# Performance work log

Hardware: AMD Instinct MI355X
Metric: run time of the kernel (lower is better)

## Reference

```python
import jax, jax.numpy as jnp
import numpy as np
import math

B, T, D, H = 4, 2048, 1024, 16
DH = D // H

def setup_inputs() -> dict:
    key = jax.random.key(0)
    ks = jax.random.split(key, 5)
    scale = 1.0 / math.sqrt(D)
    x = jax.random.normal(ks[0], (B, T, D), dtype=jnp.float32)
    Wq = jax.random.normal(ks[1], (D, D), dtype=jnp.float32) * scale
    Wk = jax.random.normal(ks[2], (D, D), dtype=jnp.float32) * scale
    Wv = jax.random.normal(ks[3], (D, D), dtype=jnp.float32) * scale
    Wo = jax.random.normal(ks[4], (D, D), dtype=jnp.float32) * scale
    mask = jnp.tril(jnp.ones((T, T), dtype=jnp.int32))  # causal, 1=keep
    return {"x": x, "mask": mask, "Wq": Wq, "Wk": Wk, "Wv": Wv, "Wo": Wo}

def reference(x, mask, Wq, Wk, Wv, Wo):
    Bx, Tx, Dx = x.shape
    # nn.Linear(bias=False): y = x @ W.T
    q = (x @ Wq.T).reshape(Bx, Tx, H, DH).transpose(0, 2, 1, 3)  # [B,H,T,dh]
    k = (x @ Wk.T).reshape(Bx, Tx, H, DH).transpose(0, 2, 1, 3)
    v = (x @ Wv.T).reshape(Bx, Tx, H, DH).transpose(0, 2, 1, 3)
    scores = jnp.einsum('bhqd,bhkd->bhqk', q, k) / math.sqrt(DH)
    m = mask[None, None, :, :]  # [1,1,T,T]
    scores = scores + (m == 0).astype(scores.dtype) * -1e9
    attn = jax.nn.softmax(scores, axis=-1)  # stable (max-subtract) like original
    out = jnp.einsum('bhqk,bhkd->bhqd', attn, v)
    out = out.transpose(0, 2, 1, 3).reshape(Bx, Tx, Dx)
    return out @ Wo.T
```

## Files before the change

kernel.cpp:

```cpp
#include <hip/hip_runtime.h>
#include <stdint.h>

#define B_  4
#define T_  2048
#define D_  1024
#define H_  16
#define DH_ 64

typedef unsigned short u16;
typedef __attribute__((ext_vector_type(8))) short bf16x8;
typedef __attribute__((ext_vector_type(8))) unsigned short u16x8;
typedef __attribute__((ext_vector_type(4))) unsigned short u16x4;
typedef __attribute__((ext_vector_type(4))) float f32x4;

#define NT_ ((size_t)B_ * T_ * D_)
#define QSCALE 0.18033688011112043f

__device__ __forceinline__ u16 f2bf(float f) {
    union { float f; uint32_t u; } v; v.f = f;
    uint32_t r = v.u + 0x7FFFu + ((v.u >> 16) & 1u);
    return (u16)(r >> 16);
}

__device__ __forceinline__ uint32_t pack2(float lo, float hi) {
    union { float f; uint32_t u; } a, b; a.f = lo; b.f = hi;
    return __builtin_amdgcn_perm(b.u, a.u, 0x07060302u);
}

__device__ __forceinline__ void gl2lds16(const u16* g, u16* l) {
    __builtin_amdgcn_global_load_lds(
        (const __attribute__((address_space(1))) unsigned int*)g,
        (__attribute__((address_space(3))) unsigned int*)l,
        16, 0, 0);
}

#define VMCNT(n) asm volatile("s_waitcnt vmcnt(" #n ")" ::: "memory")
#define SB0()    __builtin_amdgcn_sched_barrier(0)

__device__ __forceinline__ bf16x8 ldsrd(const u16* base, int row, int ks,
                                        int lq, int swzr) {
    int off = row * 128 + ks * 64 + lq * 16;
    return *(const bf16x8*)((const char*)base + (off ^ swzr));
}

__global__ __launch_bounds__(256) void cvt_x_kernel(
    const float* __restrict__ src, u16* __restrict__ dst, int n8)
{
    int i = blockIdx.x * 256 + threadIdx.x;
    if (i >= n8) return;
    f32x4 a = ((const f32x4*)src)[2 * i];
    f32x4 b = ((const f32x4*)src)[2 * i + 1];
    u16x8 o;
    o[0]=f2bf(a[0]); o[1]=f2bf(a[1]); o[2]=f2bf(a[2]); o[3]=f2bf(a[3]);
    o[4]=f2bf(b[0]); o[5]=f2bf(b[1]); o[6]=f2bf(b[2]); o[7]=f2bf(b[3]);
    ((u16x8*)dst)[i] = o;
}

__global__ __launch_bounds__(256) void cvt_w_kernel(
    const float* __restrict__ w0, const float* __restrict__ w1,
    const float* __restrict__ w2, const float* __restrict__ w3,
    u16* __restrict__ dst)
{
    const float* src = (blockIdx.y == 0) ? w0 : (blockIdx.y == 1) ? w1
                     : (blockIdx.y == 2) ? w2 : w3;
    u16* d = dst + (size_t)blockIdx.y * (D_ * D_);
    int i = blockIdx.x * 256 + threadIdx.x;
    f32x4 a = ((const f32x4*)src)[2 * i];
    f32x4 b = ((const f32x4*)src)[2 * i + 1];
    u16x8 o;
    o[0]=f2bf(a[0]); o[1]=f2bf(a[1]); o[2]=f2bf(a[2]); o[3]=f2bf(a[3]);
    o[4]=f2bf(b[0]); o[5]=f2bf(b[1]); o[6]=f2bf(b[2]); o[7]=f2bf(b[3]);
    ((u16x8*)d)[i] = o;
}

template<int OUT_MODE>
__global__ __launch_bounds__(512) void gemm8_kernel(
    const u16* __restrict__ X, const u16* __restrict__ W,
    void* __restrict__ C, int M, int N, int K)
{
    __shared__ __align__(16) u16 Ab2[2][256 * 64];
    __shared__ __align__(16) u16 Bb2[2][192 * 64];

    const int tid  = threadIdx.x;
    const int wave = tid >> 6;
    const int lane = tid & 63;
    const int lq = lane >> 4, lm = lane & 15;
    const int wm = wave >> 2;
    const int wn = wave & 3;

    const int xcd = (int)blockIdx.x & 7;
    const int idx = (int)blockIdx.x >> 3;
    const int m0 = (((xcd & 3) << 3) + (idx & 7)) << 8;
    const int n0 = (((xcd >> 2) << 3) + (idx >> 3)) * 192;

    const int srow = wave * 8 + (lane >> 3);
    const int scol = ((lane & 7) ^ (lane >> 3)) << 3;
    const u16* gA = X + (size_t)(m0 + srow) * K + scol;
    const u16* gB = W + (size_t)(n0 + srow) * K + scol;
    const size_t rK64 = (size_t)64 * K;

    const int swzr = (lm & 7) << 4;

    f32x4 acc[8][3] = {};
    bf16x8 afA[2][2], afB[2][2];
    bf16x8 bqA[3][2], bqB[3][2];
    const int NT = K >> 6;

    gl2lds16(gA,            (u16*)Ab2[0] + wave * 512);
    gl2lds16(gA + rK64,     (u16*)Ab2[0] + 4096  + wave * 512);
    gl2lds16(gA + 2 * rK64, (u16*)Ab2[0] + 8192  + wave * 512);
    gl2lds16(gA + 3 * rK64, (u16*)Ab2[0] + 12288 + wave * 512);
    gl2lds16(gB,            (u16*)Bb2[0] + wave * 512);
    gl2lds16(gB + rK64,     (u16*)Bb2[0] + 4096  + wave * 512);
    gl2lds16(gB + 2 * rK64, (u16*)Bb2[0] + 8192  + wave * 512);
    gl2lds16(gB + 64,            (u16*)Bb2[1] + wave * 512);
    gl2lds16(gB + 64 + rK64,     (u16*)Bb2[1] + 4096  + wave * 512);
    gl2lds16(gB + 64 + 2 * rK64, (u16*)Bb2[1] + 8192  + wave * 512);
    VMCNT(3);
    __builtin_amdgcn_s_barrier();
#pragma unroll
    for (int i2 = 0; i2 < 2; ++i2)
#pragma unroll
        for (int ks = 0; ks < 2; ++ks)
            afA[i2][ks] = ldsrd(Ab2[0], wm * 128 + i2 * 16 + lm, ks, lq, swzr);
#pragma unroll
    for (int j = 0; j < 3; ++j)
#pragma unroll
        for (int ks = 0; ks < 2; ++ks)
            bqA[j][ks] = ldsrd(Bb2[0], wn * 48 + j * 16 + lm, ks, lq, swzr);

    auto tile_body = [&](int t, bf16x8 (&bqU)[3][2], bf16x8 (&bqF)[3][2])
        __attribute__((always_inline)) -> void {
        const u16* Ac = Ab2[t & 1];
        const u16* An = Ab2[(t + 1) & 1];
        const u16* Bn = Bb2[(t + 1) & 1];
        u16* Abn = (u16*)Ab2[(t + 1) & 1];
        u16* Bbc = (u16*)Bb2[t & 1];
        const bool stA = (t + 1 < NT);
        const bool stB = (t + 2 < NT);
        const u16* gAs = gA + (size_t)(t + 1) * 64;
        const u16* gBs = gB + (size_t)(t + 2) * 64;

#define MFMA_PH(Q, AF, BQ)                                                  \
        __builtin_amdgcn_s_setprio(1);                                      \
        _Pragma("unroll")                                                   \
        for (int ks = 0; ks < 2; ++ks)                                      \
            _Pragma("unroll")                                               \
            for (int i2 = 0; i2 < 2; ++i2)                                  \
                _Pragma("unroll")                                           \
                for (int j = 0; j < 3; ++j)                                 \
                    acc[2 * (Q) + i2][j] =                                  \
                        __builtin_amdgcn_mfma_f32_16x16x32_bf16(            \
                            AF[i2][ks], BQ[j][ks], acc[2 * (Q) + i2][j],    \
                            0, 0, 0);                                       \
        __builtin_amdgcn_s_setprio(0);

#define RD_AF(SET, P, BASE)                                                 \
        _Pragma("unroll")                                                   \
        for (int i2 = 0; i2 < 2; ++i2)                                      \
            _Pragma("unroll")                                               \
            for (int ks = 0; ks < 2; ++ks)                                  \
                SET[i2][ks] = ldsrd(BASE,                                   \
                    wm * 128 + (2 * (P) + i2) * 16 + lm, ks, lq, swzr);

        RD_AF(afB, 1, Ac);
        if (stA) {
            gl2lds16(gAs,        Abn + wave * 512);
            gl2lds16(gAs + rK64, Abn + 4096 + wave * 512);
        }
        SB0(); __builtin_amdgcn_s_barrier(); SB0();
        MFMA_PH(0, afA, bqU); SB0();
        __builtin_amdgcn_s_barrier();

        RD_AF(afA, 2, Ac);
        if (stA) {
            gl2lds16(gAs + 2 * rK64, Abn + 8192  + wave * 512);
            gl2lds16(gAs + 3 * rK64, Abn + 12288 + wave * 512);
        }
        SB0(); __builtin_amdgcn_s_barrier(); SB0();
        MFMA_PH(1, afB, bqU); SB0();
        __builtin_amdgcn_s_barrier();

        RD_AF(afB, 3, Ac);
        if (stB) {
            gl2lds16(gBs,        Bbc + wave * 512);
            gl2lds16(gBs + rK64, Bbc + 4096 + wave * 512);
        }
        SB0(); __builtin_amdgcn_s_barrier(); SB0();
        MFMA_PH(2, afA, bqU); SB0();
        if (stB)      { VMCNT(2); }
        else if (stA) { VMCNT(0); }
        __builtin_amdgcn_s_barrier();

        if (stA) {
            RD_AF(afA, 0, An);
#pragma unroll
            for (int j = 0; j < 3; ++j)
#pragma unroll
                for (int ks = 0; ks < 2; ++ks)
                    bqF[j][ks] = ldsrd(Bn, wn * 48 + j * 16 + lm, ks, lq, swzr);
        }
        if (stB)
            gl2lds16(gBs + 2 * rK64, Bbc + 8192 + wave * 512);
        SB0(); __builtin_amdgcn_s_barrier(); SB0();
        MFMA_PH(3, afB, bqU); SB0();
        __builtin_amdgcn_s_barrier();
#undef RD_AF
#undef MFMA_PH
    };

#pragma unroll 1
    for (int tt = 0; tt < NT; tt += 2) {
        tile_body(tt,     bqA, bqB);
        tile_body(tt + 1, bqB, bqA);
    }

#pragma unroll
    for (int i = 0; i < 8; ++i)
#pragma unroll
        for (int j = 0; j < 3; ++j) {
            int rowb = m0 + wm * 128 + i * 16 + lq * 4;
            int col  = n0 + wn * 48 + j * 16 + lm;
            if (OUT_MODE == 2) {
#pragma unroll
                for (int r = 0; r < 4; ++r)
                    ((float*)C)[(size_t)(rowb + r) * N + col] = acc[i][j][r];
            } else {
                u16* Qp = (u16*)C;
                int region = col >> 10;
                int colr = col & 1023;
                if (region == 0) {
#pragma unroll
                    for (int r = 0; r < 4; ++r)
                        Qp[(size_t)(rowb + r) * D_ + colr] = f2bf(acc[i][j][r] * QSCALE);
                } else if (region == 1) {
#pragma unroll
                    for (int r = 0; r < 4; ++r)
                        (Qp + NT_)[(size_t)(rowb + r) * D_ + colr] = f2bf(acc[i][j][r]);
                } else {
                    int b = rowb >> 11, tt2 = rowb & (T_ - 1);
                    u16x4 pk;
#pragma unroll
                    for (int r = 0; r < 4; ++r) pk[r] = f2bf(acc[i][j][r]);
                    *(u16x4*)((Qp + 2 * NT_) + ((size_t)b * D_ + colr) * T_ + tt2) = pk;
                }
            }
        }
}

__global__ __launch_bounds__(256) void gemm_bt_kernel(
    const u16* __restrict__ X, const u16* __restrict__ W,
    float* __restrict__ C, int M, int N, int K)
{
    __shared__ __align__(16) u16 As[128 * 64];
    __shared__ __align__(16) u16 Bs[128 * 64];

    const int tid  = threadIdx.x;
    const int wave = tid >> 6;
    const int lane = tid & 63;
    const int lq = lane >> 4;
    const int lm = lane & 15;
    const int m0 = blockIdx.x * 128;
    const int n0 = blockIdx.y * 128;
    const int wm = (wave & 1) * 64;
    const int wn = (wave >> 1) * 64;

    f32x4 acc[4][4] = {};

    const int r0 = wave * 32 + (lane >> 3);
    const int c0 = (lane & 7) * 8;
    const u16* gA = X + (size_t)(m0 + r0) * K + c0;
    const u16* gB = W + (size_t)(n0 + r0) * K + c0;
    u16* lA = As + wave * 32 * 64;
    u16* lB = Bs + wave * 32 * 64;

    for (int k0 = 0; k0 < K; k0 += 64) {
#pragma unroll
        for (int p = 0; p < 4; ++p) {
            gl2lds16(gA + (size_t)p * 8 * K + k0, lA + p * 8 * 64);
            gl2lds16(gB + (size_t)p * 8 * K + k0, lB + p * 8 * 64);
        }
        __syncthreads();
#pragma unroll
        for (int ks = 0; ks < 2; ++ks) {
            bf16x8 af[4], bfr[4];
#pragma unroll
            for (int t = 0; t < 4; ++t)
                af[t] = *(const bf16x8*)(As + (wm + t * 16 + lm) * 64 + ks * 32 + lq * 8);
#pragma unroll
            for (int t = 0; t < 4; ++t)
                bfr[t] = *(const bf16x8*)(Bs + (wn + t * 16 + lm) * 64 + ks * 32 + lq * 8);
#pragma unroll
            for (int i = 0; i < 4; ++i)
#pragma unroll
                for (int j = 0; j < 4; ++j)
                    acc[i][j] = __builtin_amdgcn_mfma_f32_16x16x32_bf16(
                        af[i], bfr[j], acc[i][j], 0, 0, 0);
        }
        __syncthreads();
    }

#pragma unroll
    for (int i = 0; i < 4; ++i)
#pragma unroll
        for (int j = 0; j < 4; ++j) {
            int rowb = m0 + wm + i * 16 + lq * 4;
            int col  = n0 + wn + j * 16 + lm;
#pragma unroll
            for (int r = 0; r < 4; ++r)
                C[(size_t)(rowb + r) * N + col] = acc[i][j][r];
        }
}

__global__ __launch_bounds__(128) void attn_kernel(
    const u16* __restrict__ Qg, const u16* __restrict__ Kg,
    const u16* __restrict__ Vtg, u16* __restrict__ Og)
{
    __shared__ __align__(16) u16 Pl[2 * 64 * 40];
    __shared__ __align__(16) float Oc[16 * 64 * 4];
    __shared__ __align__(16) float Lc[4 * 64];

    const int tid  = threadIdx.x;
    const int wave = tid >> 6;
    const int lane = tid & 63;
    const int lq = lane >> 4, lm = lane & 15;
    const int id = blockIdx.x;
    const int xs = id & 7;
    const int k8 = id >> 3;
    const int bh = xs + 8 * (k8 & 7);
    const int pi = k8 >> 3;
    const int b = bh >> 4, h = bh & 15;

    const size_t batchoff = (size_t)b * T_ * D_;
    const size_t headoff  = (size_t)h * DH_;
    const size_t vbase    = (size_t)bh * DH_ * T_;

    u16* pw = Pl + wave * 64 * 40;

#pragma unroll 1
    for (int ph = 0; ph < 2; ++ph) {
        const int qj  = ph ? (31 - pi) : pi;
        const int qw  = qj * 64;
        const int ktd = qj >> 1;
        const int odd = qj & 1;

        bf16x8 aq[4][2];
#pragma unroll
        for (int qf = 0; qf < 4; ++qf) {
            const u16* qrow = Qg + batchoff + (size_t)(qw + qf * 16 + lm) * D_ + headoff;
            aq[qf][0] = *(const bf16x8*)(qrow + lq * 8);
            aq[qf][1] = *(const bf16x8*)(qrow + 32 + lq * 8);
        }

        f32x4 oaccT[4][4] = {};
        float l_lane[4] = {0.f, 0.f, 0.f, 0.f};

#pragma unroll 1
        for (int kt = wave; kt <= ktd; kt += 2) {
            const bool diag = (kt == ktd);
            const int ksmax = diag ? (odd ? 3 : 1) : 3;

#pragma unroll
            for (int c = 0; c < 4; ++c) {
                if (c <= ksmax) {
#pragma unroll
                    for (int t = 0; t < 2; ++t) {
                        const int mt = 2 * c + t;
                        const u16* krow = Kg + batchoff
                            + (size_t)(kt * 128 + mt * 16 + lm) * D_ + headoff;
                        bf16x8 kf0 = *(const bf16x8*)(krow + lq * 8);
                        bf16x8 kf1 = *(const bf16x8*)(krow + 32 + lq * 8);
                        f32x4 s[4];
#pragma unroll
                        for (int qf = 0; qf < 4; ++qf) {
                            s[qf] = f32x4{0.f, 0.f, 0.f, 0.f};
                            s[qf] = __builtin_amdgcn_mfma_f32_16x16x32_bf16(
                                kf0, aq[qf][0], s[qf], 0, 0, 0);
                            s[qf] = __builtin_amdgcn_mfma_f32_16x16x32_bf16(
                                kf1, aq[qf][1], s[qf], 0, 0, 0);
                        }
                        if (diag) {
                            int keyb = kt * 128 + mt * 16 + lq * 4;
#pragma unroll
                            for (int qf = 0; qf < 4; ++qf) {
                                int query = qw + qf * 16 + lm;
#pragma unroll
                                for (int r = 0; r < 4; ++r)
                                    if (keyb + r > query) s[qf][r] = -1e9f;
                            }
                        }
#pragma unroll
                        for (int qf = 0; qf < 4; ++qf) {
                            float p0 = __builtin_amdgcn_exp2f(s[qf][0]);
                            float p1 = __builtin_amdgcn_exp2f(s[qf][1]);
                            float p2 = __builtin_amdgcn_exp2f(s[qf][2]);
                            float p3 = __builtin_amdgcn_exp2f(s[qf][3]);
                            l_lane[qf] += (p0 + p1) + (p2 + p3);
                            uint2 d; d.x = pack2(p0, p1); d.y = pack2(p2, p3);
                            *(uint2*)(pw + (qf * 16 + lm) * 40 + t * 16 + lq * 4) = d;
                        }
                    }

                    bf16x8 pf[4];
#pragma unroll
                    for (int qf = 0; qf < 4; ++qf)
                        pf[qf] = *(const bf16x8*)(pw + (qf * 16 + lm) * 40 + lq * 8);
#pragma unroll
                    for (int mo = 0; mo < 4; ++mo) {
                        const u16* vrow = Vtg + vbase
                            + (size_t)(mo * 16 + lm) * T_ + kt * 128 + c * 32;
                        bf16x8 vf = *(const bf16x8*)(vrow + lq * 8);
#pragma unroll
                        for (int qf = 0; qf < 4; ++qf)
                            oaccT[qf][mo] = __builtin_amdgcn_mfma_f32_16x16x32_bf16(
                                vf, pf[qf], oaccT[qf][mo], 0, 0, 0);
                    }
                }
            }
        }

        if (wave == 1) {
#pragma unroll
            for (int qf = 0; qf < 4; ++qf) {
#pragma unroll
                for (int mo = 0; mo < 4; ++mo)
                    *(f32x4*)&Oc[((qf * 4 + mo) * 64 + lane) * 4] = oaccT[qf][mo];
                Lc[qf * 64 + lane] = l_lane[qf];
            }
        }
        __syncthreads();
        if (wave == 0) {
#pragma unroll
            for (int qf = 0; qf < 4; ++qf) {
#pragma unroll
                for (int mo = 0; mo < 4; ++mo) {
                    f32x4 o = *(const f32x4*)&Oc[((qf * 4 + mo) * 64 + lane) * 4];
#pragma unroll
                    for (int r = 0; r < 4; ++r) oaccT[qf][mo][r] += o[r];
                }
                l_lane[qf] += Lc[qf * 64 + lane];
            }
#pragma unroll
            for (int qf = 0; qf < 4; ++qf) {
                float l = l_lane[qf];
                l += __shfl_xor(l, 16, 64);
                l += __shfl_xor(l, 32, 64);
                float inv = 1.0f / l;
                int row = qw + qf * 16 + lm;
                u16* obase = Og + batchoff + (size_t)row * D_ + headoff;
#pragma unroll
                for (int mo = 0; mo < 4; ++mo) {
                    uint2 d;
                    d.x = pack2(oaccT[qf][mo][0] * inv, oaccT[qf][mo][1] * inv);
                    d.y = pack2(oaccT[qf][mo][2] * inv, oaccT[qf][mo][3] * inv);
                    *(uint2*)(obase + mo * 16 + lq * 4) = d;
                }
            }
        }
        __syncthreads();
    }
}

extern "C" void kernel_launch(void* const* d_in, const int* in_sizes, int n_in,
                              void* d_out, int out_size, void* d_ws, size_t ws_size,
                              hipStream_t stream)
{
    const float* x  = (const float*)d_in[0];
    const float* Wq = (const float*)d_in[2];
    const float* Wk = (const float*)d_in[3];
    const float* Wv = (const float*)d_in[4];
    const float* Wo = (const float*)d_in[5];

    const size_t DD = (size_t)D_ * D_;
    u16* Qb  = (u16*)d_ws;
    u16* Kb  = Qb + NT_;
    u16* Vb  = Kb + NT_;
    u16* Ob  = Vb + NT_;
    u16* xb  = Ob + NT_;
    u16* wb  = xb + NT_;

    const int M = B_ * T_;

    cvt_x_kernel<<<dim3((int)(NT_ / 8 / 256)), 256, 0, stream>>>(x, xb, (int)(NT_ / 8));
    cvt_w_kernel<<<dim3((int)(DD / 8 / 256), 4), 256, 0, stream>>>(Wq, Wk, Wv, Wo, wb);

    gemm8_kernel<3><<<dim3((M / 256) * (3 * D_ / 192)), 512, 0, stream>>>(
        xb, wb, Qb, M, 3 * D_, D_);

    attn_kernel<<<dim3(1024), 128, 0, stream>>>(Qb, Kb, Vb, Ob);

    gemm_bt_kernel<<<dim3(M / 128, D_ / 128), 256, 0, stream>>>(
        Ob, wb + 3 * DD, (float*)d_out, M, D_, D_);
}
```

Measured before the change: 271.3 us.

## Give each attention block one query tile and reuse P LDS for reduction

The attention kernel now launches one block per 64-query tile (2048 blocks) instead of pairing a light and a heavy causal tile per block. Blocks are ordered heaviest-first so the scheduler can balance load. The separate shared-memory buffers for the cross-wave O/l reduction are removed, and the reduction reuses the P staging buffer in two halves with a swizzled index, which shrinks LDS per block so more blocks can be resident. In exchange there are more block launches, repeated Q setup per block, and extra barriers in the reduction.

```diff
diff --git a/kernel.cpp b/kernel.cpp
--- a/kernel.cpp
+++ b/kernel.cpp
@@ -317,8 +317,6 @@
     const u16* __restrict__ Vtg, u16* __restrict__ Og)
 {
     __shared__ __align__(16) u16 Pl[2 * 64 * 40];
-    __shared__ __align__(16) float Oc[16 * 64 * 4];
-    __shared__ __align__(16) float Lc[4 * 64];
 
     const int tid  = threadIdx.x;
     const int wave = tid >> 6;
@@ -326,9 +324,8 @@
     const int lq = lane >> 4, lm = lane & 15;
     const int id = blockIdx.x;
     const int xs = id & 7;
-    const int k8 = id >> 3;
-    const int bh = xs + 8 * (k8 & 7);
-    const int pi = k8 >> 3;
+    const int bh = xs + 8 * ((id >> 3) & 7);
+    const int qj = 31 - (id >> 6);
     const int b = bh >> 4, h = bh & 15;
 
     const size_t batchoff = (size_t)b * T_ * D_;
@@ -337,127 +334,145 @@
 
     u16* pw = Pl + wave * 64 * 40;
 
+    const int qw  = qj * 64;
+    const int ktd = qj >> 1;
+    const int odd = qj & 1;
+
+    bf16x8 aq[4][2];
+#pragma unroll
+    for (int qf = 0; qf < 4; ++qf) {
+        const u16* qrow = Qg + batchoff + (size_t)(qw + qf * 16 + lm) * D_ + headoff;
+        aq[qf][0] = *(const bf16x8*)(qrow + lq * 8);
+        aq[qf][1] = *(const bf16x8*)(qrow + 32 + lq * 8);
+    }
+
+    f32x4 oaccT[4][4] = {};
+    float l_lane[4] = {0.f, 0.f, 0.f, 0.f};
+
 #pragma unroll 1
-    for (int ph = 0; ph < 2; ++ph) {
-        const int qj  = ph ? (31 - pi) : pi;
-        const int qw  = qj * 64;
-        const int ktd = qj >> 1;
-        const int odd = qj & 1;
-
-        bf16x8 aq[4][2];
-#pragma unroll
-        for (int qf = 0; qf < 4; ++qf) {
-            const u16* qrow = Qg + batchoff + (size_t)(qw + qf * 16 + lm) * D_ + headoff;
-            aq[qf][0] = *(const bf16x8*)(qrow + lq * 8);
-            aq[qf][1] = *(const bf16x8*)(qrow + 32 + lq * 8);
-        }
-
-        f32x4 oaccT[4][4] = {};
-        float l_lane[4] = {0.f, 0.f, 0.f, 0.f};
-
-#pragma unroll 1
-        for (int kt = wave; kt <= ktd; kt += 2) {
-            const bool diag = (kt == ktd);
-            const int ksmax = diag ? (odd ? 3 : 1) : 3;
-
-#pragma unroll
-            for (int c = 0; c < 4; ++c) {
-                if (c <= ksmax) {
-#pragma unroll
-                    for (int t = 0; t < 2; ++t) {
-                        const int mt = 2 * c + t;
-                        const u16* krow = Kg + batchoff
-                            + (size_t)(kt * 128 + mt * 16 + lm) * D_ + headoff;
-                        bf16x8 kf0 = *(const bf16x8*)(krow + lq * 8);
-                        bf16x8 kf1 = *(const bf16x8*)(krow + 32 + lq * 8);
-                        f32x4 s[4];
+    for (int kt = wave; kt <= ktd; kt += 2) {
+        const bool diag = (kt == ktd);
+        const int ksmax = diag ? (odd ? 3 : 1) : 3;
+
+#pragma unroll
+        for (int c = 0; c < 4; ++c) {
+            if (c <= ksmax) {
+#pragma unroll
+                for (int t = 0; t < 2; ++t) {
+                    const int mt = 2 * c + t;
+                    const u16* krow = Kg + batchoff
+                        + (size_t)(kt * 128 + mt * 16 + lm) * D_ + headoff;
+                    bf16x8 kf0 = *(const bf16x8*)(krow + lq * 8);
+                    bf16x8 kf1 = *(const bf16x8*)(krow + 32 + lq * 8);
+                    f32x4 s[4];
+#pragma unroll
+                    for (int qf = 0; qf < 4; ++qf) {
+                        s[qf] = f32x4{0.f, 0.f, 0.f, 0.f};
+                        s[qf] = __builtin_amdgcn_mfma_f32_16x16x32_bf16(
+                            kf0, aq[qf][0], s[qf], 0, 0, 0);
+                        s[qf] = __builtin_amdgcn_mfma_f32_16x16x32_bf16(
+                            kf1, aq[qf][1], s[qf], 0, 0, 0);
+                    }
+                    if (diag) {
+                        int keyb = kt * 128 + mt * 16 + lq * 4;
 #pragma unroll
                         for (int qf = 0; qf < 4; ++qf) {
-                            s[qf] = f32x4{0.f, 0.f, 0.f, 0.f};
-                            s[qf] = __builtin_amdgcn_mfma_f32_16x16x32_bf16(
-                                kf0, aq[qf][0], s[qf], 0, 0, 0);
-                            s[qf] = __builtin_amdgcn_mfma_f32_16x16x32_bf16(
-                                kf1, aq[qf][1], s[qf], 0, 0, 0);
-                        }
-                        if (diag) {
-                            int keyb = kt * 128 + mt * 16 + lq * 4;
-#pragma unroll
-                            for (int qf = 0; qf < 4; ++qf) {
-                                int query = qw + qf * 16 + lm;
-#pragma unroll
-                                for (int r = 0; r < 4; ++r)
-                                    if (keyb + r > query) s[qf][r] = -1e9f;
-                            }
-                        }
-#pragma unroll
-                        for (int qf = 0; qf < 4; ++qf) {
-                            float p0 = __builtin_amdgcn_exp2f(s[qf][0]);
-                            float p1 = __builtin_amdgcn_exp2f(s[qf][1]);
-                            float p2 = __builtin_amdgcn_exp2f(s[qf][2]);
-                            float p3 = __builtin_amdgcn_exp2f(s[qf][3]);
-                            l_lane[qf] += (p0 + p1) + (p2 + p3);
-                            uint2 d; d.x = pack2(p0, p1); d.y = pack2(p2, p3);
-                            *(uint2*)(pw + (qf * 16 + lm) * 40 + t * 16 + lq * 4) = d;
+                            int query = qw + qf * 16 + lm;
+#pragma unroll
+                            for (int r = 0; r < 4; ++r)
+                                if (keyb + r > query) s[qf][r] = -1e9f;
                         }
                     }
-
-                    bf16x8 pf[4];
-#pragma unroll
-                    for (int qf = 0; qf < 4; ++qf)
-                        pf[qf] = *(const bf16x8*)(pw + (qf * 16 + lm) * 40 + lq * 8);
-#pragma unroll
-                    for (int mo = 0; mo < 4; ++mo) {
-                        const u16* vrow = Vtg + vbase
-                            + (size_t)(mo * 16 + lm) * T_ + kt * 128 + c * 32;
-                        bf16x8 vf = *(const bf16x8*)(vrow + lq * 8);
-#pragma unroll
-                        for (int qf = 0; qf < 4; ++qf)
-                            oaccT[qf][mo] = __builtin_amdgcn_mfma_f32_16x16x32_bf16(
-                                vf, pf[qf], oaccT[qf][mo], 0, 0, 0);
+#pragma unroll
+                    for (int qf = 0; qf < 4; ++qf) {
+                        float p0 = __builtin_amdgcn_exp2f(s[qf][0]);
+                        float p1 = __builtin_amdgcn_exp2f(s[qf][1]);
+                        float p2 = __builtin_amdgcn_exp2f(s[qf][2]);
+                        float p3 = __builtin_amdgcn_exp2f(s[qf][3]);
+                        l_lane[qf] += (p0 + p1) + (p2 + p3);
+                        uint2 d; d.x = pack2(p0, p1); d.y = pack2(p2, p3);
+                        *(uint2*)(pw + (qf * 16 + lm) * 40 + t * 16 + lq * 4) = d;
                     }
                 }
-            }
-        }
-
-        if (wave == 1) {
-#pragma unroll
-            for (int qf = 0; qf < 4; ++qf) {
-#pragma unroll
-                for (int mo = 0; mo < 4; ++mo)
-                    *(f32x4*)&Oc[((qf * 4 + mo) * 64 + lane) * 4] = oaccT[qf][mo];
-                Lc[qf * 64 + lane] = l_lane[qf];
-            }
-        }
-        __syncthreads();
-        if (wave == 0) {
-#pragma unroll
-            for (int qf = 0; qf < 4; ++qf) {
+
+                bf16x8 pf[4];
+#pragma unroll
+                for (int qf = 0; qf < 4; ++qf)
+                    pf[qf] = *(const bf16x8*)(pw + (qf * 16 + lm) * 40 + lq * 8);
 #pragma unroll
                 for (int mo = 0; mo < 4; ++mo) {
-                    f32x4 o = *(const f32x4*)&Oc[((qf * 4 + mo) * 64 + lane) * 4];
-#pragma unroll
-                    for (int r = 0; r < 4; ++r) oaccT[qf][mo][r] += o[r];
-                }
-                l_lane[qf] += Lc[qf * 64 + lane];
-            }
-#pragma unroll
-            for (int qf = 0; qf < 4; ++qf) {
-                float l = l_lane[qf];
-                l += __shfl_xor(l, 16, 64);
-                l += __shfl_xor(l, 32, 64);
-                float inv = 1.0f / l;
-                int row = qw + qf * 16 + lm;
-                u16* obase = Og + batchoff + (size_t)row * D_ + headoff;
-#pragma unroll
-                for (int mo = 0; mo < 4; ++mo) {
-                    uint2 d;
-                    d.x = pack2(oaccT[qf][mo][0] * inv, oaccT[qf][mo][1] * inv);
-                    d.y = pack2(oaccT[qf][mo][2] * inv, oaccT[qf][mo][3] * inv);
-                    *(uint2*)(obase + mo * 16 + lq * 4) = d;
+                    const u16* vrow = Vtg + vbase
+                        + (size_t)(mo * 16 + lm) * T_ + kt * 128 + c * 32;
+                    bf16x8 vf = *(const bf16x8*)(vrow + lq * 8);
+#pragma unroll
+                    for (int qf = 0; qf < 4; ++qf)
+                        oaccT[qf][mo] = __builtin_amdgcn_mfma_f32_16x16x32_bf16(
+                            vf, pf[qf], oaccT[qf][mo], 0, 0, 0);
                 }
             }
         }
-        __syncthreads();
+    }
+
+    float* Cf = (float*)Pl;
+    const int cswz = (lane ^ (lane >> 3)) * 4;
+    __syncthreads();
+    if (wave == 1) {
+#pragma unroll
+        for (int qf = 0; qf < 2; ++qf)
+#pragma unroll
+            for (int mo = 0; mo < 4; ++mo)
+                *(f32x4*)&Cf[(qf * 4 + mo) * 256 + cswz] = oaccT[qf][mo];
+#pragma unroll
+        for (int qf = 0; qf < 4; ++qf)
+            Cf[2048 + qf * 64 + lane] = l_lane[qf];
+    }
+    __syncthreads();
+    if (wave == 0) {
+#pragma unroll
+        for (int qf = 0; qf < 2; ++qf)
+#pragma unroll
+            for (int mo = 0; mo < 4; ++mo) {
+                f32x4 o = *(const f32x4*)&Cf[(qf * 4 + mo) * 256 + cswz];
+#pragma unroll
+                for (int r = 0; r < 4; ++r) oaccT[qf][mo][r] += o[r];
+            }
+#pragma unroll
+        for (int qf = 0; qf < 4; ++qf) l_lane[qf] += Cf[2048 + qf * 64 + lane];
+    }
+    __syncthreads();
+    if (wave == 1) {
+#pragma unroll
+        for (int qf = 2; qf < 4; ++qf)
+#pragma unroll
+            for (int mo = 0; mo < 4; ++mo)
+                *(f32x4*)&Cf[((qf - 2) * 4 + mo) * 256 + cswz] = oaccT[qf][mo];
+    }
+    __syncthreads();
+    if (wave == 0) {
+#pragma unroll
+        for (int qf = 2; qf < 4; ++qf)
+#pragma unroll
+            for (int mo = 0; mo < 4; ++mo) {
+                f32x4 o = *(const f32x4*)&Cf[((qf - 2) * 4 + mo) * 256 + cswz];
+#pragma unroll
+                for (int r = 0; r < 4; ++r) oaccT[qf][mo][r] += o[r];
+            }
+#pragma unroll
+        for (int qf = 0; qf < 4; ++qf) {
+            float l = l_lane[qf];
+            l += __shfl_xor(l, 16, 64);
+            l += __shfl_xor(l, 32, 64);
+            float inv = 1.0f / l;
+            int row = qw + qf * 16 + lm;
+            u16* obase = Og + batchoff + (size_t)row * D_ + headoff;
+#pragma unroll
+            for (int mo = 0; mo < 4; ++mo) {
+                uint2 d;
+                d.x = pack2(oaccT[qf][mo][0] * inv, oaccT[qf][mo][1] * inv);
+                d.y = pack2(oaccT[qf][mo][2] * inv, oaccT[qf][mo][3] * inv);
+                *(uint2*)(obase + mo * 16 + lq * 4) = d;
+            }
+        }
     }
 }
 
@@ -487,7 +502,7 @@
     gemm8_kernel<3><<<dim3((M / 256) * (3 * D_ / 192)), 512, 0, stream>>>(
         xb, wb, Qb, M, 3 * D_, D_);
 
-    attn_kernel<<<dim3(1024), 128, 0, stream>>>(Qb, Kb, Vb, Ob);
+    attn_kernel<<<dim3(2048), 128, 0, stream>>>(Qb, Kb, Vb, Ob);
 
     gemm_bt_kernel<<<dim3(M / 128, D_ / 128), 256, 0, stream>>>(
         Ob, wb + 3 * DD, (float*)d_out, M, D_, D_);
```

After: 267.8 us. Within noise of the previous version (-1.3%).
